# Kernel optimization log

Hardware: AMD Instinct MI355X
Metric: run time of the kernel (lower is better)

Reference implementation:

```python
import jax, jax.numpy as jnp
import numpy as np

RADIUS = 0.1
NSAMPLE = 32


def ball_query(xyz, new_xyz, radius, nsample):
    """xyz:(B,N,3), new_xyz:(B,P,3) -> idx:(B,P,nsample) int32.
    Semantics of PointNet++ CUDA ball_query: first `nsample` points (in index
    order) within `radius`; remaining slots padded with the first found index
    (0 if no point is within radius)."""
    d2 = jnp.sum((new_xyz[:, :, None, :] - xyz[:, None, :, :]) ** 2, axis=-1)  # (B,P,N)
    mask = d2 < radius * radius
    cnt = jnp.cumsum(mask, axis=-1) - 1               # rank of each hit
    valid = mask & (cnt < nsample)
    first = jnp.argmax(mask, axis=-1)                 # first in-ball index (0 if none)
    B, P, N = d2.shape
    pos = jnp.where(valid, cnt, nsample)              # invalid -> dump slot
    buf = jnp.broadcast_to(first[..., None], (B, P, nsample + 1))
    j = jnp.broadcast_to(jnp.arange(N)[None, None, :], (B, P, N))
    b = jnp.arange(B)[:, None, None]
    p = jnp.arange(P)[None, :, None]
    buf = buf.at[b, p, pos].set(j)
    return buf[..., :nsample].astype(jnp.int32)


def setup_inputs() -> dict:
    key = jax.random.key(0)
    k1, k2, k3 = jax.random.split(key, 3)
    xyz = jax.random.uniform(k1, (2, 16384, 3), dtype=jnp.float32)
    new_xyz = jax.random.uniform(k2, (2, 4096, 3), dtype=jnp.float32)
    features = jax.random.normal(k3, (2, 64, 16384), dtype=jnp.float32)
    return {"xyz": xyz, "new_xyz": new_xyz, "features": features}


def reference(xyz, new_xyz, features):
    idx = ball_query(xyz, new_xyz, RADIUS, NSAMPLE)              # (B,P,S)
    grouped_xyz = jax.vmap(lambda x, i: x[i])(xyz, idx)          # (B,P,S,3)
    grouped_xyz = jnp.transpose(grouped_xyz, (0, 3, 1, 2))       # (B,3,P,S)
    grouped_xyz = grouped_xyz - jnp.transpose(new_xyz, (0, 2, 1))[..., None]
    grouped_feat = jax.vmap(lambda f, i: f[:, i])(features, idx) # (B,C,P,S)
    return jnp.concatenate([grouped_xyz, grouped_feat], axis=1)  # (B,3+C,P,S)
```

## Files before the change

### kernel.cpp

```cpp
#include <hip/hip_runtime.h>
#include <hip/hip_bf16.h>
#include <climits>

#define BATCH   2
#define NPTS    16384
#define NQ      4096
#define CFEAT   64
#define NS      32
#define R2      0.01f
#define COUT    (3 + CFEAT)
#define GDIM    10
#define NCELL   (GDIM * GDIM * GDIM)
#define NWORDS  (NPTS / 32)

#define FEATT_BYTES ((size_t)BATCH * NPTS * CFEAT * sizeof(unsigned short))
#define PXYZJ_BYTES ((size_t)BATCH * NPTS * sizeof(float4))
#define OFF_CNT    0
#define OFF_FILL   (2 * NCELL)
#define OFF_CSTART (4 * NCELL)
#define GRID_INTS  (4 * NCELL + 2 * (NCELL + 1))

__device__ __forceinline__ int cell_of(float x, float y, float z) {
    int cx = (int)(x * GDIM); cx = cx < 0 ? 0 : (cx > GDIM - 1 ? GDIM - 1 : cx);
    int cy = (int)(y * GDIM); cy = cy < 0 ? 0 : (cy > GDIM - 1 ? GDIM - 1 : cy);
    int cz = (int)(z * GDIM); cz = cz < 0 ? 0 : (cz > GDIM - 1 ? GDIM - 1 : cz);
    return (cz * GDIM + cy) * GDIM + cx;
}

__device__ __forceinline__ unsigned short f2bf(float f) {
    unsigned b = __float_as_uint(f);
    return (unsigned short)((b + 0x7FFFu + ((b >> 16) & 1u)) >> 16);
}

__global__ __launch_bounds__(256) void prep1_kernel(
    const float* __restrict__ feat, unsigned short* __restrict__ featT16,
    const float* __restrict__ xyz, int* __restrict__ cnt)
{
    __shared__ float tile[64][65];
    if (blockIdx.x < 512) {
        const int b    = blockIdx.x >> 8;
        const int n0   = (blockIdx.x & 255) * 64;
        const int lane = threadIdx.x & 63;
        const int grp  = threadIdx.x >> 6;
        const float* fb = feat + (size_t)b * CFEAT * NPTS;
        #pragma unroll
        for (int k = 0; k < 16; ++k) {
            const int c = grp * 16 + k;
            tile[c][lane] = fb[(size_t)c * NPTS + n0 + lane];
        }
        __syncthreads();
        unsigned short* db = featT16 + ((size_t)b * NPTS + n0) * CFEAT;
        #pragma unroll
        for (int k = 0; k < 8; ++k) {
            const int e   = threadIdx.x + 256 * k;
            const int row = e >> 5;
            const int c2  = e & 31;
            ushort2 v;
            v.x = f2bf(tile[2 * c2][row]);
            v.y = f2bf(tile[2 * c2 + 1][row]);
            ((ushort2*)(db + (size_t)row * CFEAT))[c2] = v;
        }
    } else {
        const int g = (blockIdx.x - 512) * 256 + threadIdx.x;
        const int b = g >> 14;
        const int c = cell_of(xyz[g*3], xyz[g*3+1], xyz[g*3+2]);
        atomicAdd(&cnt[b * NCELL + c], 1);
    }
}

__global__ __launch_bounds__(256) void prep2_kernel(
    const float* __restrict__ xyz, const int* __restrict__ cnt,
    int* __restrict__ fill, int* __restrict__ cstart,
    float4* __restrict__ pxyzj)
{
    __shared__ int scs[2 * NCELL];
    const int tid  = threadIdx.x;
    const int lane = tid & 63;

    if (tid < 128) {
        const int b = tid >> 6;
        int c16[16];
        int tot = 0;
        #pragma unroll
        for (int k = 0; k < 16; ++k) {
            const int i = lane * 16 + k;
            c16[k] = (i < NCELL) ? cnt[b * NCELL + i] : 0;
            tot += c16[k];
        }
        int ex = tot;
        #pragma unroll
        for (int off = 1; off < 64; off <<= 1) {
            const int u = __shfl_up(ex, off);
            if (lane >= off) ex += u;
        }
        ex -= tot;
        int run = ex;
        #pragma unroll
        for (int k = 0; k < 16; ++k) {
            const int i = lane * 16 + k;
            if (i < NCELL) scs[b * NCELL + i] = run;
            run += c16[k];
        }
    }
    __syncthreads();

    if (blockIdx.x == 0) {
        for (int i = tid; i < 2 * (NCELL + 1); i += 256) {
            const int b  = i / (NCELL + 1);
            const int ci = i - b * (NCELL + 1);
            cstart[i] = (ci == NCELL) ? NPTS : scs[b * NCELL + ci];
        }
    }

    const int g = blockIdx.x * 256 + tid;
    const int b = g >> 14;
    const int j = g & (NPTS - 1);
    const float x = xyz[g*3], y = xyz[g*3+1], z = xyz[g*3+2];
    const int c = cell_of(x, y, z);
    const int pos = atomicAdd(&fill[b * NCELL + c], 1);
    pxyzj[b * NPTS + scs[b * NCELL + c] + pos] =
        make_float4(x, y, z, __int_as_float(j));
}

__global__ __launch_bounds__(256) void qg_fused(
    const float* __restrict__ xyz,
    const float* __restrict__ new_xyz,
    const int* __restrict__ cstart,
    const float4* __restrict__ pxyzj,
    const unsigned short* __restrict__ featT16,
    float* __restrict__ out)
{
    const int tid  = threadIdx.x;
    const int wave = tid >> 6;
    const int lane = tid & 63;
    const int q    = (blockIdx.x << 2) + wave;
    const int b    = q >> 12;
    const int p    = q & (NQ - 1);

    __shared__ __align__(16) unsigned char smem[4 * 2176];
    unsigned char* wbase = smem + wave * 2176;
    unsigned int* hmask  = (unsigned int*)wbase;
    int* idx_s           = (int*)(wbase + 2048);

    {
        uint4 z; z.x = 0; z.y = 0; z.z = 0; z.w = 0;
        ((uint4*)hmask)[lane * 2]     = z;
        ((uint4*)hmask)[lane * 2 + 1] = z;
    }

    const float qx = new_xyz[q * 3 + 0];
    const float qy = new_xyz[q * 3 + 1];
    const float qz = new_xyz[q * 3 + 2];
    const float* xb = xyz + (size_t)b * NPTS * 3;
    const int* cs = cstart + b * (NCELL + 1);
    const float4* pb = pxyzj + (size_t)b * NPTS;

    int qcx = (int)(qx * GDIM); qcx = qcx < 0 ? 0 : (qcx > GDIM-1 ? GDIM-1 : qcx);
    int qcy = (int)(qy * GDIM); qcy = qcy < 0 ? 0 : (qcy > GDIM-1 ? GDIM-1 : qcy);
    int qcz = (int)(qz * GDIM); qcz = qcz < 0 ? 0 : (qcz > GDIM-1 ? GDIM-1 : qcz);
    const int x0 = qcx > 0 ? qcx - 1 : 0;
    const int x1 = qcx < GDIM-1 ? qcx + 1 : GDIM-1;
    const int y0 = qcy > 0 ? qcy - 1 : 0;
    const int y1 = qcy < GDIM-1 ? qcy + 1 : GDIM-1;
    const int z0 = qcz > 0 ? qcz - 1 : 0;
    const int z1 = qcz < GDIM-1 ? qcz + 1 : GDIM-1;
    const int ny  = y1 - y0 + 1;
    const int nyz = ny * (z1 - z0 + 1);

    int sv = 0, ev = 0;
    if (lane < nyz) {
        const int gzi = (ny == 3) ? ((lane * 86) >> 8) : (lane >> 1);
        const int gyi = lane - gzi * ny;
        const int crow = ((z0 + gzi) * GDIM + (y0 + gyi)) * GDIM;
        sv = cs[crow + x0];
        ev = cs[crow + x1 + 1];
    }
    __builtin_amdgcn_wave_barrier();

    for (int r = 0; r < nyz; ++r) {
        const int s = __shfl(sv, r);
        const int e = __shfl(ev, r);
        for (int pos = s; pos < e; pos += 64) {
            const int i = pos + lane;
            const bool inr = i < e;
            const float4 pt = pb[inr ? i : 0];
            const float dx = pt.x - qx;
            const float dy = pt.y - qy;
            const float dz = pt.z - qz;
            if (inr && (dx*dx + dy*dy + dz*dz < R2)) {
                const int j = __float_as_int(pt.w);
                atomicOr(&hmask[j >> 5], 1u << (j & 31));
            }
        }
    }
    __builtin_amdgcn_wave_barrier();

    int K;
    {
        unsigned int w[8];
        const uint4 a = ((const uint4*)hmask)[lane * 2];
        const uint4 c = ((const uint4*)hmask)[lane * 2 + 1];
        w[0] = a.x; w[1] = a.y; w[2] = a.z; w[3] = a.w;
        w[4] = c.x; w[5] = c.y; w[6] = c.z; w[7] = c.w;

        int cnt8 = 0;
        #pragma unroll
        for (int k = 0; k < 8; ++k) cnt8 += __popc(w[k]);

        int pfx = cnt8;
        #pragma unroll
        for (int off = 1; off < 64; off <<= 1) {
            const int u = __shfl_up(pfx, off);
            if (lane >= off) pfx += u;
        }
        K = __shfl(pfx, 63);
        pfx -= cnt8;

        if (pfx < NS && cnt8 > 0) {
            int r = pfx;
            #pragma unroll
            for (int k = 0; k < 8; ++k) {
                unsigned int m = w[k];
                while (m && r < NS) {
                    const int bit = __builtin_ctz(m);
                    idx_s[r] = lane * 256 + k * 32 + bit;
                    m &= m - 1;
                    ++r;
                }
            }
        }
        __builtin_amdgcn_wave_barrier();
        if (lane < NS && lane >= K) {
            idx_s[lane] = (K > 0) ? idx_s[0] : 0;
        }
        __builtin_amdgcn_wave_barrier();
    }

    const int sm = lane >> 1;
    const int h  = lane & 1;
    const int jrow = idx_s[sm];
    const uint4* bptr = (const uint4*)(featT16 +
        ((size_t)b * NPTS + jrow) * CFEAT + (h << 5));
    const uint4 ga = bptr[0];
    const uint4 gb = bptr[1];
    const uint4 gc = bptr[2];
    const uint4 gd = bptr[3];

    const size_t cstride = (size_t)NQ * NS;
    const size_t out_q   = ((size_t)b * COUT * NQ + (size_t)p) * NS;

    if (lane < NS) {
        const int j = idx_s[lane];
        out[out_q + 0*cstride + lane] = xb[j*3+0] - qx;
        out[out_q + 1*cstride + lane] = xb[j*3+1] - qy;
        out[out_q + 2*cstride + lane] = xb[j*3+2] - qz;
    }

    float* fob = out + out_q + (size_t)(3 + (h << 5)) * cstride + sm;
    const unsigned comps[16] = {ga.x, ga.y, ga.z, ga.w,
                                gb.x, gb.y, gb.z, gb.w,
                                gc.x, gc.y, gc.z, gc.w,
                                gd.x, gd.y, gd.z, gd.w};
    #pragma unroll
    for (int kk = 0; kk < 16; ++kk) {
        const unsigned u = comps[kk];
        fob[(size_t)(2*kk)     * cstride] = __uint_as_float(u << 16);
        fob[(size_t)(2*kk + 1) * cstride] = __uint_as_float(u & 0xFFFF0000u);
    }
}

__global__ __launch_bounds__(256) void qg_linear(
    const float* __restrict__ xyz, const float* __restrict__ new_xyz,
    const float* __restrict__ feat, float* __restrict__ out)
{
    const int wave = threadIdx.x >> 6;
    const int lane = threadIdx.x & 63;
    const int bp   = blockIdx.x * 4 + wave;
    const int b    = bp >> 12;
    const int p    = bp & (NQ - 1);
    __shared__ int idx_s[4][NS];
    const float qx = new_xyz[bp*3+0], qy = new_xyz[bp*3+1], qz = new_xyz[bp*3+2];
    const float* xb = xyz + (size_t)b * NPTS * 3;
    int cnt = 0;
    const unsigned long long below = (1ull << lane) - 1ull;
    for (int base = 0; base < NPTS; base += 64) {
        const int j = base + lane;
        const float dx = xb[j*3+0]-qx, dy = xb[j*3+1]-qy, dz = xb[j*3+2]-qz;
        const bool hit = dx*dx+dy*dy+dz*dz < R2;
        const unsigned long long m = __ballot(hit);
        if (hit) {
            const int slot = cnt + __popcll(m & below);
            if (slot < NS) idx_s[wave][slot] = j;
        }
        cnt += __popcll(m);
        if (cnt >= NS) break;
    }
    __builtin_amdgcn_wave_barrier();
    if (cnt < NS) {
        const int first = (cnt > 0) ? idx_s[wave][0] : 0;
        if (lane >= cnt && lane < NS) idx_s[wave][lane] = first;
    }
    __builtin_amdgcn_wave_barrier();
    const size_t cstride = (size_t)NQ * NS;
    const size_t out_q = ((size_t)b * COUT * NQ + (size_t)p) * NS;
    if (lane < NS) {
        const int j = idx_s[wave][lane];
        out[out_q + 0*cstride + lane] = xb[j*3+0] - qx;
        out[out_q + 1*cstride + lane] = xb[j*3+1] - qy;
        out[out_q + 2*cstride + lane] = xb[j*3+2] - qz;
    }
    const float* fb = feat + (size_t)b * CFEAT * NPTS;
    const int s = lane & 31, half = lane >> 5;
    const int j = idx_s[wave][s];
    #pragma unroll 8
    for (int c = half; c < CFEAT; c += 2)
        out[out_q + (size_t)(3 + c) * cstride + s] = fb[(size_t)c * NPTS + j];
}

extern "C" void kernel_launch(void* const* d_in, const int* in_sizes, int n_in,
                              void* d_out, int out_size, void* d_ws, size_t ws_size,
                              hipStream_t stream) {
    const float* xyz     = (const float*)d_in[0];
    const float* new_xyz = (const float*)d_in[1];
    const float* feat    = (const float*)d_in[2];
    float* out = (float*)d_out;

    const size_t need_full = FEATT_BYTES + PXYZJ_BYTES + (size_t)GRID_INTS * sizeof(int);

    if (ws_size >= need_full) {
        unsigned short* featT16 = (unsigned short*)d_ws;
        float4* pxyzj = (float4*)((char*)d_ws + FEATT_BYTES);
        int* gi = (int*)((char*)d_ws + FEATT_BYTES + PXYZJ_BYTES);
        int* cnt    = gi + OFF_CNT;
        int* fill   = gi + OFF_FILL;
        int* cstart = gi + OFF_CSTART;

        hipMemsetAsync(cnt, 0, 4 * NCELL * sizeof(int), stream);
        prep1_kernel<<<512 + (BATCH * NPTS) / 256, 256, 0, stream>>>(feat, featT16, xyz, cnt);
        prep2_kernel<<<(BATCH * NPTS) / 256, 256, 0, stream>>>(xyz, cnt, fill, cstart, pxyzj);
        qg_fused<<<(BATCH * NQ) / 4, 256, 0, stream>>>(
            xyz, new_xyz, cstart, pxyzj, featT16, out);
    } else {
        qg_linear<<<(BATCH * NQ) / 4, 256, 0, stream>>>(xyz, new_xyz, feat, out);
    }
}
```

Measured before the change: 113.1 us.

## Merge memset and two prep kernels into one cooperative kernel with grid syncs

Replaces the memset plus the prep1 and prep2 launches with a single cooperative kernel of 256 blocks. It uses grid.sync() to order the count zeroing, the histogram and feature transpose, and the scan and scatter phases. The aim is to remove two launch gaps and the memset. In exchange, each block now does more work serially, and the cooperative launch and grid-wide barriers add their own cost.

```diff
diff --git a/kernel.cpp b/kernel.cpp
--- a/kernel.cpp
+++ b/kernel.cpp
@@ -1,6 +1,9 @@
 #include <hip/hip_runtime.h>
 #include <hip/hip_bf16.h>
+#include <hip/hip_cooperative_groups.h>
 #include <climits>
+
+namespace cg = cooperative_groups;
 
 #define BATCH   2
 #define NPTS    16384
@@ -32,17 +35,41 @@
     return (unsigned short)((b + 0x7FFFu + ((b >> 16) & 1u)) >> 16);
 }
 
-__global__ __launch_bounds__(256) void prep1_kernel(
+__global__ __launch_bounds__(256) void prep_coop(
     const float* __restrict__ feat, unsigned short* __restrict__ featT16,
-    const float* __restrict__ xyz, int* __restrict__ cnt)
+    const float* __restrict__ xyz, int* __restrict__ cnt,
+    int* __restrict__ fill, int* __restrict__ cstart,
+    float4* __restrict__ pxyzj)
 {
-    __shared__ float tile[64][65];
-    if (blockIdx.x < 512) {
-        const int b    = blockIdx.x >> 8;
-        const int n0   = (blockIdx.x & 255) * 64;
-        const int lane = threadIdx.x & 63;
-        const int grp  = threadIdx.x >> 6;
+    cg::grid_group grid = cg::this_grid();
+    __shared__ __align__(16) unsigned char smem[64 * 65 * sizeof(float)];
+    float (*tile)[65] = (float(*)[65])smem;
+    int* scs          = (int*)smem;
+
+    const int tid  = threadIdx.x;
+    const int lane = tid & 63;
+
+    {
+        const int gid = blockIdx.x * 256 + tid;
+        if (gid < 4 * NCELL) cnt[gid] = 0;
+    }
+    grid.sync();
+
+    if (tid < 128) {
+        const int g = blockIdx.x * 128 + tid;
+        const int b = g >> 14;
+        const int c = cell_of(xyz[g*3], xyz[g*3+1], xyz[g*3+2]);
+        atomicAdd(&cnt[b * NCELL + c], 1);
+    }
+
+    #pragma unroll
+    for (int it = 0; it < 2; ++it) {
+        const int t  = (blockIdx.x << 1) + it;
+        const int b  = t >> 8;
+        const int n0 = (t & 255) * 64;
+        const int grp = tid >> 6;
         const float* fb = feat + (size_t)b * CFEAT * NPTS;
+        if (it) __syncthreads();
         #pragma unroll
         for (int k = 0; k < 16; ++k) {
             const int c = grp * 16 + k;
@@ -52,7 +79,7 @@
         unsigned short* db = featT16 + ((size_t)b * NPTS + n0) * CFEAT;
         #pragma unroll
         for (int k = 0; k < 8; ++k) {
-            const int e   = threadIdx.x + 256 * k;
+            const int e   = tid + 256 * k;
             const int row = e >> 5;
             const int c2  = e & 31;
             ushort2 v;
@@ -60,22 +87,8 @@
             v.y = f2bf(tile[2 * c2 + 1][row]);
             ((ushort2*)(db + (size_t)row * CFEAT))[c2] = v;
         }
-    } else {
-        const int g = (blockIdx.x - 512) * 256 + threadIdx.x;
-        const int b = g >> 14;
-        const int c = cell_of(xyz[g*3], xyz[g*3+1], xyz[g*3+2]);
-        atomicAdd(&cnt[b * NCELL + c], 1);
-    }
-}
-
-__global__ __launch_bounds__(256) void prep2_kernel(
-    const float* __restrict__ xyz, const int* __restrict__ cnt,
-    int* __restrict__ fill, int* __restrict__ cstart,
-    float4* __restrict__ pxyzj)
-{
-    __shared__ int scs[2 * NCELL];
-    const int tid  = threadIdx.x;
-    const int lane = tid & 63;
+    }
+    grid.sync();
 
     if (tid < 128) {
         const int b = tid >> 6;
@@ -112,14 +125,16 @@
         }
     }
 
-    const int g = blockIdx.x * 256 + tid;
-    const int b = g >> 14;
-    const int j = g & (NPTS - 1);
-    const float x = xyz[g*3], y = xyz[g*3+1], z = xyz[g*3+2];
-    const int c = cell_of(x, y, z);
-    const int pos = atomicAdd(&fill[b * NCELL + c], 1);
-    pxyzj[b * NPTS + scs[b * NCELL + c] + pos] =
-        make_float4(x, y, z, __int_as_float(j));
+    if (tid < 128) {
+        const int g = blockIdx.x * 128 + tid;
+        const int b = g >> 14;
+        const int j = g & (NPTS - 1);
+        const float x = xyz[g*3], y = xyz[g*3+1], z = xyz[g*3+2];
+        const int c = cell_of(x, y, z);
+        const int pos = atomicAdd(&fill[b * NCELL + c], 1);
+        pxyzj[b * NPTS + scs[b * NCELL + c] + pos] =
+            make_float4(x, y, z, __int_as_float(j));
+    }
 }
 
 __global__ __launch_bounds__(256) void qg_fused(
@@ -335,9 +350,10 @@
         int* fill   = gi + OFF_FILL;
         int* cstart = gi + OFF_CSTART;
 
-        hipMemsetAsync(cnt, 0, 4 * NCELL * sizeof(int), stream);
-        prep1_kernel<<<512 + (BATCH * NPTS) / 256, 256, 0, stream>>>(feat, featT16, xyz, cnt);
-        prep2_kernel<<<(BATCH * NPTS) / 256, 256, 0, stream>>>(xyz, cnt, fill, cstart, pxyzj);
+        void* args[] = {(void*)&feat, (void*)&featT16, (void*)&xyz,
+                        (void*)&cnt, (void*)&fill, (void*)&cstart, (void*)&pxyzj};
+        hipLaunchCooperativeKernel((void*)prep_coop, dim3(256), dim3(256),
+                                   args, 0, stream);
         qg_fused<<<(BATCH * NQ) / 4, 256, 0, stream>>>(
             xyz, new_xyz, cstart, pxyzj, featT16, out);
     } else {
```

Result: slower. 176.8 us (+56.3%).
